# Kernel optimization log

Measured on AMD Instinct MI355X. Metric: run time of the kernel, lower is better.

Reference implementation:

```python
import jax, jax.numpy as jnp
import numpy as np

FRAME_LEN, HOP, FFT_LEN = 400, 160, 512
PREEMPH = 0.97
MEL_FLOOR = 1.192092955078125e-07


def _hz_to_mel(f):
    return 2595.0 * np.log10(1.0 + f / 700.0)


def _build_mel_filters():
    # mirrors mel_filter_bank(256, 80, 20, 8000, 16000) with filter_freqs = mel_freqs (as in source)
    num_freq_bins, num_mel = 256, 80
    mel_min, mel_max = _hz_to_mel(20.0), _hz_to_mel(8000.0)
    filter_freqs = np.linspace(mel_min, mel_max, num_mel + 2)
    fft_bin_width = 16000.0 / (num_freq_bins * 2)
    fft_freqs = _hz_to_mel(fft_bin_width * np.arange(num_freq_bins))
    filter_diff = np.diff(filter_freqs)
    slopes = filter_freqs[None, :] - fft_freqs[:, None]  # (256, 82)
    down = -slopes[:, :-2] / filter_diff[:-1]
    up = slopes[:, 2:] / filter_diff[1:]
    fb = np.maximum(0.0, np.minimum(down, up))  # (256, 80)
    return np.pad(fb, ((0, 1), (0, 0))).astype(np.float32)  # (257, 80)


def _build_window():
    n = np.arange(FRAME_LEN)
    hann = 0.5 * (1.0 - np.cos(2.0 * np.pi * n / (FRAME_LEN - 1)))  # periodic=False
    return (hann ** 0.85).astype(np.float32)


def setup_inputs() -> dict:
    key = jax.random.key(0)
    k1, = jax.random.split(key, 1)
    B, N = 32, 480000
    raw_speech = jax.random.normal(k1, (B, N), dtype=jnp.float32)
    mask = jnp.ones((B, N), dtype=jnp.float32)
    return {
        "raw_speech": raw_speech,
        "mask": mask,
        "mel_filters": jnp.asarray(_build_mel_filters()),
        "window": jnp.asarray(_build_window()),
    }


def reference(raw_speech, mask, mel_filters, window):
    stride, pad_mult, padding_value = 2, 2, 1.0
    wav = raw_speech * 32768.0  # * 2**15
    B, N = wav.shape
    num_frames = 1 + (N - FRAME_LEN) // HOP
    # vectorized framing (replaces per-frame python loop)
    idx = jnp.arange(num_frames)[:, None] * HOP + jnp.arange(FRAME_LEN)[None, :]
    frames = wav[:, idx]      # (B, F, 400)
    mframes = mask[:, idx]    # (B, F, 400)
    # remove DC offset
    frames = frames - frames.mean(axis=-1, keepdims=True)
    # preemphasis (first sample scaled by 1-p, matching the source)
    frames = jnp.concatenate(
        [frames[..., :1] * (1.0 - PREEMPH), frames[..., 1:] - PREEMPH * frames[..., :-1]],
        axis=-1,
    )
    frames = frames * window * mframes
    spec = jnp.fft.rfft(frames, n=FFT_LEN, axis=-1)  # (B, F, 257) zero-padded fft
    power = jnp.abs(spec) ** 2.0
    feats = jnp.log(jnp.maximum(power @ mel_filters, MEL_FLOOR))  # (B, F, 80)
    # per-utterance normalization over frames (unbiased variance)
    mean = feats.mean(axis=1, keepdims=True)
    var = feats.var(axis=1, keepdims=True, ddof=1)
    feats = (feats - mean) / jnp.sqrt(var + 1e-7)
    # stride-stacking
    rem = num_frames % stride
    F2 = num_frames - rem
    feats = feats[:, :F2].reshape(B, F2 // stride, 80 * stride)
    # pad frames dim to multiple of pad_to_multiple_of with padding_value
    n = feats.shape[1]
    P = (pad_mult - n % pad_mult) % pad_mult
    input_features = jnp.pad(feats, ((0, 0), (0, P), (0, 0)), constant_values=padding_value)
    attention_mask = jnp.concatenate(
        [jnp.ones((B, n), jnp.int32), jnp.zeros((B, P), jnp.int32)], axis=1
    )
    return input_features, attention_mask
```

## Files before the change

### kernel.cpp

```cpp
#include <hip/hip_runtime.h>
#include <math.h>

#define NFRAMES 2998
#define BATCH 32
#define NSAMP 480000
#define NMEL 80
#define NBINS 257
#define ROWS 1500
#define COLS 160
#define MEL_FLOOR 1.192092955078125e-07f
#define PI_F 3.14159265358979323846f
#define SCHUNKS 32

#define SW2(a) ((a) ^ (5 * (((a) >> 4) & 3)))

template<int NS>
__device__ inline void r4pass2(const float2* __restrict__ s, float2* __restrict__ d, int j)
{
    const int k = j & (NS - 1);
    float2 va = s[SW2(j)];
    float2 vb = s[SW2(j + 64)];
    float2 vc = s[SW2(j + 128)];
    float2 vd = s[SW2(j + 192)];

    float t1r, t1i, t2r, t2i, t3r, t3i;
    if (NS == 1) {
        t1r = vb.x; t1i = vb.y; t2r = vc.x; t2i = vc.y; t3r = vd.x; t3i = vd.y;
    } else {
        float s1, c1;
        __sincosf((-PI_F / (2.0f * (float)NS)) * (float)k, &s1, &c1);
        float c2 = c1 * c1 - s1 * s1, s2 = 2.0f * c1 * s1;
        float c3 = c1 * c2 - s1 * s2, s3 = c1 * s2 + s1 * c2;
        t1r = vb.x * c1 - vb.y * s1; t1i = vb.x * s1 + vb.y * c1;
        t2r = vc.x * c2 - vc.y * s2; t2i = vc.x * s2 + vc.y * c2;
        t3r = vd.x * c3 - vd.y * s3; t3i = vd.x * s3 + vd.y * c3;
    }
    float e0r = va.x + t2r, e0i = va.y + t2i;
    float e1r = va.x - t2r, e1i = va.y - t2i;
    float e2r = t1r + t3r,  e2i = t1i + t3i;
    float e3r = t1r - t3r,  e3i = t1i - t3i;
    const int i0 = 4 * j - 3 * k;
    d[SW2(i0)]          = make_float2(e0r + e2r, e0i + e2i);
    d[SW2(i0 + NS)]     = make_float2(e1r + e3i, e1i - e3r);
    d[SW2(i0 + 2*NS)]   = make_float2(e0r - e2r, e0i - e2i);
    d[SW2(i0 + 3*NS)]   = make_float2(e1r - e3i, e1i + e3r);
}

__global__ __launch_bounds__(256) void k_ranges(const float* __restrict__ fil,
                                                int* __restrict__ rlo, int* __restrict__ rlen)
{
    const int m    = blockIdx.x * 4 + (threadIdx.x >> 6);
    const int lane = threadIdx.x & 63;
    int lo = NBINS, hi = -1;
    for (int f = lane; f < NBINS; f += 64) {
        if (fil[f * NMEL + m] > 0.f) { lo = min(lo, f); hi = max(hi, f); }
    }
    #pragma unroll
    for (int o = 1; o < 64; o <<= 1) {
        lo = min(lo, __shfl_xor(lo, o, 64));
        hi = max(hi, __shfl_xor(hi, o, 64));
    }
    if (lane == 0) {
        rlo[m]  = (hi < 0) ? 0 : lo;
        rlen[m] = (hi < 0) ? 0 : (hi - lo + 1);
    }
}

__global__ __launch_bounds__(256) void k_frames(
    const float* __restrict__ raw, const float* __restrict__ mask,
    const float* __restrict__ fil, const float* __restrict__ win,
    const int* __restrict__ rlo, const int* __restrict__ rlen,
    float* __restrict__ feats)
{
    __shared__ float2 A2[4][256];
    __shared__ __align__(16) union {
        struct { float x[896]; float mk[896]; } in;
        float2 c2[4][256];
    } U;
    __shared__ float s_pow[4][NBINS];

    const int tid  = threadIdx.x;
    const int wv   = tid >> 6;
    const int lane = tid & 63;
    const int b    = blockIdx.y;
    const int fr0  = blockIdx.x * 4;
    const long sbase = (long)b * NSAMP + (long)fr0 * 160;
    const int  valid = NSAMP - fr0 * 160;

    for (int i4 = tid; i4 < 220; i4 += 256) {
        float4 xv = make_float4(0.f, 0.f, 0.f, 0.f);
        float4 mv = make_float4(0.f, 0.f, 0.f, 0.f);
        if (i4 * 4 + 4 <= valid) {
            xv = *(const float4*)(raw  + sbase + i4 * 4);
            mv = *(const float4*)(mask + sbase + i4 * 4);
        }
        xv.x *= 32768.f; xv.y *= 32768.f; xv.z *= 32768.f; xv.w *= 32768.f;
        *(float4*)&U.in.x[i4 * 4]  = xv;
        *(float4*)&U.in.mk[i4 * 4] = mv;
    }
    __syncthreads();

    float part = 0.f;
    for (int i = lane; i < 400; i += 64) part += U.in.x[wv * 160 + i];
    #pragma unroll
    for (int o = 1; o < 64; o <<= 1) part += __shfl_xor(part, o, 64);
    const float fmean = part * (1.0f / 400.0f);

    {
        const int l = lane;
        float ys[8];
        if (l < 50) {
            const float* xp = &U.in.x[wv * 160 + 8 * l];
            const float* mp = &U.in.mk[wv * 160 + 8 * l];
            float4 x0 = *(const float4*)xp,        x1 = *(const float4*)(xp + 4);
            float4 m0 = *(const float4*)mp,        m1 = *(const float4*)(mp + 4);
            float4 w0 = *(const float4*)(win + 8 * l), w1 = *(const float4*)(win + 8 * l + 4);
            float xm1 = (l > 0) ? xp[-1] : 0.f;
            float xs[8] = {x0.x, x0.y, x0.z, x0.w, x1.x, x1.y, x1.z, x1.w};
            float ms[8] = {m0.x, m0.y, m0.z, m0.w, m1.x, m1.y, m1.z, m1.w};
            float wf[8] = {w0.x, w0.y, w0.z, w0.w, w1.x, w1.y, w1.z, w1.w};
            #pragma unroll
            for (int e = 0; e < 8; ++e) {
                float xc = xs[e];
                float xprev = e ? xs[e - 1] : xm1;
                float y = (8 * l + e == 0) ? 0.03f * (xc - fmean)
                                           : (xc - 0.97f * xprev - 0.03f * fmean);
                ys[e] = y * wf[e] * ms[e];
            }
        } else {
            #pragma unroll
            for (int e = 0; e < 8; ++e) ys[e] = 0.f;
        }
        __syncthreads();
        #pragma unroll
        for (int d = 0; d < 4; ++d) {
            A2[wv][SW2(4 * l + d)] = make_float2(ys[2 * d], ys[2 * d + 1]);
        }
    }

    r4pass2<1 >(&A2[wv][0],   &U.c2[wv][0], lane);
    r4pass2<4 >(&U.c2[wv][0], &A2[wv][0],   lane);
    r4pass2<16>(&A2[wv][0],   &U.c2[wv][0], lane);
    r4pass2<64>(&U.c2[wv][0], &A2[wv][0],   lane);

    #pragma unroll
    for (int q = 0; q < 4; ++q) {
        int k  = lane + 64 * q;
        int a  = k & 255;
        int b2 = (256 - k) & 255;
        float2 za = A2[wv][SW2(a)];
        float2 zb = A2[wv][SW2(b2)];
        float Er  = 0.5f * (za.x + zb.x), Ei = 0.5f * (za.y - zb.y);
        float Or_ = 0.5f * (za.y + zb.y), Oi = 0.5f * (zb.x - za.x);
        float sk, ck;
        __sincosf((-PI_F / 256.0f) * (float)k, &sk, &ck);
        float Xr = Er + ck * Or_ - sk * Oi;
        float Xi = Ei + ck * Oi + sk * Or_;
        s_pow[wv][k] = Xr * Xr + Xi * Xi;
    }
    if (lane == 0) {
        float2 z0 = A2[wv][SW2(0)];
        float Xr = z0.x - z0.y;
        s_pow[wv][256] = Xr * Xr;
    }
    __syncthreads();

    for (int p = tid; p < 4 * NMEL; p += 256) {
        int g = p / NMEL, m = p - NMEL * g;
        int fr = fr0 + g;
        if (fr >= NFRAMES) continue;
        int lo = rlo[m], len = rlen[m];
        float acc = 0.f;
        for (int i = 0; i < len; ++i) {
            int f = lo + i;
            acc = fmaf(s_pow[g][f], fil[f * NMEL + m], acc);
        }
        feats[((long)b * NFRAMES + fr) * NMEL + m] = __logf(fmaxf(acc, MEL_FLOOR));
    }
}

__global__ __launch_bounds__(256) void k_stats1(const float* __restrict__ feats,
                                                float* __restrict__ partials)
{
    const int b  = blockIdx.x;
    const int ch = blockIdx.y;
    const int t  = threadIdx.x;
    const int fr0 = (NFRAMES * ch) / SCHUNKS;
    const int fr1 = (NFRAMES * (ch + 1)) / SCHUNKS;

    float4 s  = make_float4(0.f, 0.f, 0.f, 0.f);
    float4 s2 = make_float4(0.f, 0.f, 0.f, 0.f);
    if (t < 240) {
        const int c = t % 20;
        const int r = t / 20;
        const float4* base = (const float4*)(feats + (long)b * NFRAMES * NMEL);
        for (int fr = fr0 + r; fr < fr1; fr += 12) {
            float4 v = base[(long)fr * 20 + c];
            s.x += v.x; s.y += v.y; s.z += v.z; s.w += v.w;
            s2.x += v.x * v.x; s2.y += v.y * v.y; s2.z += v.z * v.z; s2.w += v.w * v.w;
        }
    }
    __shared__ float4 ls[240], ls2[240];
    if (t < 240) { ls[t] = s; ls2[t] = s2; }
    __syncthreads();
    if (t < 20) {
        float4 a = ls[t], a2 = ls2[t];
        for (int r = 1; r < 12; ++r) {
            float4 u = ls[r * 20 + t], u2 = ls2[r * 20 + t];
            a.x += u.x; a.y += u.y; a.z += u.z; a.w += u.w;
            a2.x += u2.x; a2.y += u2.y; a2.z += u2.z; a2.w += u2.w;
        }
        float4* p = (float4*)(partials + (long)(b * SCHUNKS + ch) * 2 * NMEL);
        p[t]      = a;
        p[20 + t] = a2;
    }
}

__global__ __launch_bounds__(256) void k_out(const float* __restrict__ feats,
                                             const float* __restrict__ partials,
                                             float* __restrict__ out)
{
    const int b = blockIdx.y;
    const int t = threadIdx.x;
    __shared__ float sm[NMEL], sr[NMEL];

    if (t < NMEL) {
        const float* p = partials + (long)b * SCHUNKS * 2 * NMEL;
        float s = 0.f, s2 = 0.f;
        #pragma unroll 4
        for (int ch = 0; ch < SCHUNKS; ++ch) {
            s  += p[ch * 2 * NMEL + t];
            s2 += p[ch * 2 * NMEL + NMEL + t];
        }
        float mean = s * (1.0f / NFRAMES);
        float var  = (s2 - s * s * (1.0f / NFRAMES)) * (1.0f / (NFRAMES - 1));
        sm[t] = mean;
        sr[t] = rsqrtf(var + 1e-7f);
    }
    __syncthreads();

    const int tot4 = ROWS * COLS / 4;
    float* ob = out + (long)b * ROWS * COLS;
    for (int i = blockIdx.x * 256 + t; i < tot4; i += gridDim.x * 256) {
        int e = i * 4;
        int r = e / COLS, c = e % COLS;
        float4 o;
        if (r == ROWS - 1) {
            o = make_float4(1.f, 1.f, 1.f, 1.f);
        } else {
            int fr = 2 * r + (c >= NMEL);
            int m  = c % NMEL;
            const float4 f = *(const float4*)(feats + ((long)b * NFRAMES + fr) * NMEL + m);
            o.x = (f.x - sm[m])     * sr[m];
            o.y = (f.y - sm[m + 1]) * sr[m + 1];
            o.z = (f.z - sm[m + 2]) * sr[m + 2];
            o.w = (f.w - sm[m + 3]) * sr[m + 3];
        }
        *(float4*)(ob + e) = o;
    }

    if (blockIdx.x == 0) {
        float* omask = out + (long)BATCH * ROWS * COLS + (long)b * ROWS;
        for (int i = t; i < ROWS; i += 256) {
            omask[i] = (i == ROWS - 1) ? 0.0f : 1.0f;
        }
    }
}

extern "C" void kernel_launch(void* const* d_in, const int* in_sizes, int n_in,
                              void* d_out, int out_size, void* d_ws, size_t ws_size,
                              hipStream_t stream)
{
    const float* raw  = (const float*)d_in[0];
    const float* mask = (const float*)d_in[1];
    const float* fil  = (const float*)d_in[2];
    const float* win  = (const float*)d_in[3];
    float* out = (float*)d_out;

    float* feats    = (float*)d_ws;
    float* partials = feats + (long)BATCH * NFRAMES * NMEL;
    int*   rlo      = (int*)(partials + (long)BATCH * SCHUNKS * 2 * NMEL);
    int*   rlen     = rlo + NMEL;

    k_ranges<<<20, 256, 0, stream>>>(fil, rlo, rlen);

    dim3 g1((NFRAMES + 3) / 4, BATCH);
    k_frames<<<g1, 256, 0, stream>>>(raw, mask, fil, win, rlo, rlen, feats);

    dim3 gs(BATCH, SCHUNKS);
    k_stats1<<<gs, 256, 0, stream>>>(feats, partials);

    dim3 go(16, BATCH);
    k_out<<<go, 256, 0, stream>>>(feats, partials, out);
}
```

Measured before the change: 273.3 us.

## Compact mel filter to fixed-width band layout cached in shared memory

The ranges kernel now writes a compacted, transposed filter table of width MAXW=20 per mel band. The frames kernel loads this table and the band starts into LDS and runs a fixed, unrolled 20-tap dot product. This replaces the variable-length loop that read the filter from global memory with strided access. The fixed width assumes no mel band spans more than 20 bins; a wider band would be silently truncated. The power buffer is padded with zeros so reads past bin 256 stay in bounds.

```diff
diff --git a/kernel.cpp b/kernel.cpp
--- a/kernel.cpp
+++ b/kernel.cpp
@@ -11,6 +11,7 @@
 #define MEL_FLOOR 1.192092955078125e-07f
 #define PI_F 3.14159265358979323846f
 #define SCHUNKS 32
+#define MAXW 20
 
 #define SW2(a) ((a) ^ (5 * (((a) >> 4) & 3)))
 
@@ -47,7 +48,8 @@
 }
 
 __global__ __launch_bounds__(256) void k_ranges(const float* __restrict__ fil,
-                                                int* __restrict__ rlo, int* __restrict__ rlen)
+                                                int* __restrict__ rlo,
+                                                float* __restrict__ filT)
 {
     const int m    = blockIdx.x * 4 + (threadIdx.x >> 6);
     const int lane = threadIdx.x & 63;
@@ -60,16 +62,19 @@
         lo = min(lo, __shfl_xor(lo, o, 64));
         hi = max(hi, __shfl_xor(hi, o, 64));
     }
-    if (lane == 0) {
-        rlo[m]  = (hi < 0) ? 0 : lo;
-        rlen[m] = (hi < 0) ? 0 : (hi - lo + 1);
+    if (hi < 0) { lo = 0; hi = -1; }
+    if (lane == 0) rlo[m] = lo;
+    if (lane < MAXW) {
+        int f = lo + lane;
+        float v = (f <= hi && f < NBINS) ? fil[f * NMEL + m] : 0.f;
+        filT[lane * NMEL + m] = v;
     }
 }
 
 __global__ __launch_bounds__(256) void k_frames(
     const float* __restrict__ raw, const float* __restrict__ mask,
-    const float* __restrict__ fil, const float* __restrict__ win,
-    const int* __restrict__ rlo, const int* __restrict__ rlen,
+    const float* __restrict__ filT, const float* __restrict__ win,
+    const int* __restrict__ rlo,
     float* __restrict__ feats)
 {
     __shared__ float2 A2[4][256];
@@ -77,7 +82,9 @@
         struct { float x[896]; float mk[896]; } in;
         float2 c2[4][256];
     } U;
-    __shared__ float s_pow[4][NBINS];
+    __shared__ float s_pow[4][280];
+    __shared__ float s_filT[MAXW * NMEL];
+    __shared__ int   s_rlo[NMEL];
 
     const int tid  = threadIdx.x;
     const int wv   = tid >> 6;
@@ -86,6 +93,11 @@
     const int fr0  = blockIdx.x * 4;
     const long sbase = (long)b * NSAMP + (long)fr0 * 160;
     const int  valid = NSAMP - fr0 * 160;
+
+    for (int i4 = tid; i4 < MAXW * NMEL / 4; i4 += 256) {
+        *(float4*)&s_filT[i4 * 4] = *(const float4*)&filT[i4 * 4];
+    }
+    if (tid < NMEL) s_rlo[tid] = rlo[tid];
 
     for (int i4 = tid; i4 < 220; i4 += 256) {
         float4 xv = make_float4(0.f, 0.f, 0.f, 0.f);
@@ -163,17 +175,18 @@
         float Xr = z0.x - z0.y;
         s_pow[wv][256] = Xr * Xr;
     }
+    if (lane < 23) s_pow[wv][257 + lane] = 0.f;
     __syncthreads();
 
     for (int p = tid; p < 4 * NMEL; p += 256) {
         int g = p / NMEL, m = p - NMEL * g;
         int fr = fr0 + g;
         if (fr >= NFRAMES) continue;
-        int lo = rlo[m], len = rlen[m];
+        int lo = s_rlo[m];
         float acc = 0.f;
-        for (int i = 0; i < len; ++i) {
-            int f = lo + i;
-            acc = fmaf(s_pow[g][f], fil[f * NMEL + m], acc);
+        #pragma unroll
+        for (int i = 0; i < MAXW; ++i) {
+            acc = fmaf(s_pow[g][lo + i], s_filT[i * NMEL + m], acc);
         }
         feats[((long)b * NFRAMES + fr) * NMEL + m] = __logf(fmaxf(acc, MEL_FLOOR));
     }
@@ -279,13 +292,13 @@
 
     float* feats    = (float*)d_ws;
     float* partials = feats + (long)BATCH * NFRAMES * NMEL;
-    int*   rlo      = (int*)(partials + (long)BATCH * SCHUNKS * 2 * NMEL);
-    int*   rlen     = rlo + NMEL;
-
-    k_ranges<<<20, 256, 0, stream>>>(fil, rlo, rlen);
+    float* filT     = partials + (long)BATCH * SCHUNKS * 2 * NMEL;
+    int*   rlo      = (int*)(filT + MAXW * NMEL);
+
+    k_ranges<<<20, 256, 0, stream>>>(fil, rlo, filT);
 
     dim3 g1((NFRAMES + 3) / 4, BATCH);
-    k_frames<<<g1, 256, 0, stream>>>(raw, mask, fil, win, rlo, rlen, feats);
+    k_frames<<<g1, 256, 0, stream>>>(raw, mask, filT, win, rlo, feats);
 
     dim3 gs(BATCH, SCHUNKS);
     k_stats1<<<gs, 256, 0, stream>>>(feats, partials);
```

New measurement: 249.2 us. 8.8% less time.
